# Optimization experiments

Measured on AMD Instinct MI355X. Metric: run time of the kernel, lower is better.

## Reference

```python
import jax, jax.numpy as jnp
import numpy as np

D = 8        # input_path_dim (number of driving channels / base vector fields)
N = 256      # cde_state_dim
H = 512      # vf_hidden_dim
B = 4096     # batch of evaluation points (vmapped calls)
P = D * (D - 1) // 2            # number of depth-2 Lyndon brackets (i<j)
M = D + P                       # total brackets = depth-2 Lyndon basis size
_II, _JJ = np.triu_indices(D, k=1)   # Lyndon words (i,j), i<j


def _mlp_fields(h, W1, b1, W2, b2, W3, b3, Wo, bo):
    # eqx.nn.MLP(in=N, out=D*N, width=H, depth=3, softplus hidden, tanh final)
    x = jax.nn.softplus(W1 @ h + b1)
    x = jax.nn.softplus(W2 @ x + b2)
    x = jax.nn.softplus(W3 @ x + b3)
    return jnp.tanh(Wo @ x + bo).reshape(D, N)   # V_i(h), i=1..D


def setup_inputs() -> dict:
    key = jax.random.key(0)
    ks = jax.random.split(key, 10)

    def lin(kw, kb, out_dim, in_dim):
        lim = 1.0 / np.sqrt(in_dim)
        W = jax.random.uniform(kw, (out_dim, in_dim), minval=-lim, maxval=lim, dtype=jnp.float32)
        b = jax.random.uniform(kb, (out_dim,), minval=-lim, maxval=lim, dtype=jnp.float32)
        return W, b

    W1, b1 = lin(ks[0], ks[1], H, N)
    W2, b2 = lin(ks[2], ks[3], H, H)
    W3, b3 = lin(ks[4], ks[5], H, H)
    Wo, bo = lin(ks[6], ks[7], D * N, H)
    h = jax.random.normal(ks[8], (B, N), dtype=jnp.float32)
    primitive_signature = jax.random.normal(ks[9], (B, M), dtype=jnp.float32) * 0.1
    return {
        "h": h, "primitive_signature": primitive_signature,
        "W1": W1, "b1": b1, "W2": W2, "b2": b2,
        "W3": W3, "b3": b3, "Wo": Wo, "bo": bo,
    }


def reference(h, primitive_signature, W1, b1, W2, b2, W3, b3, Wo, bo):
    def single(hv, sig):
        F = lambda y: _mlp_fields(y, W1, b1, W2, b2, W3, b3, Wo, bo)  # [D, N]
        V = F(hv)                                                      # level-1 brackets V_i(h)
        # J[k, i] = DV_i(h) @ V_k(h); one jvp per base-field direction
        J = jax.vmap(lambda v: jax.jvp(F, (hv,), (v,))[1])(V)          # [D, D, N]
        # Lyndon lift, depth 2: [V_i, V_j](h) = DV_j V_i - DV_i V_j, i<j
        lvl2 = J[_II, _JJ] - J[_JJ, _II]                               # [P, N]
        brackets = jnp.concatenate([V, lvl2], axis=0)                  # [M, N]
        # log-ODE contraction against primitive log-signature coefficients
        return jnp.einsum("mn,m->n", brackets, sig)                    # [N]

    return jax.vmap(single)(h, primitive_signature)                    # [B, N]
```

## Files before the change

### kernel.cpp

```cpp
#include <hip/hip_runtime.h>
#include <hip/hip_bf16.h>
#include <math.h>

#define MM 36

typedef _Float16 f16;
typedef __attribute__((ext_vector_type(8))) _Float16 f16x8;
typedef __attribute__((ext_vector_type(4))) _Float16 f16x4;
typedef __attribute__((ext_vector_type(4))) float f32x4;

enum { EPI_NONE = 0, EPI_SP = 1, EPI_TANH = 2, EPI_GATE = 3 };

__device__ __forceinline__ void gl_lds16(const f16* g, f16* l) {
    __builtin_amdgcn_global_load_lds(
        (const __attribute__((address_space(1))) void*)g,
        (__attribute__((address_space(3))) void*)l, 16, 0, 0);
}

template <int EPI, int BM, int BN, int TPB, int WN>
__global__ __launch_bounds__(TPB, 4) void gemm16(
    const f16* __restrict__ A, int lda, long aZ,
    const f16* __restrict__ W, int ldw, long wZ,
    const float* __restrict__ bias,
    void* __restrict__ C0v, int ldc, long cZ,
    const f16* __restrict__ G,
    int K, int cshift)
{
    constexpr int WM = TPB / 64 / WN;
    constexpr int FM = BM / (WM * 16);
    constexpr int FN = BN / (WN * 16);
    constexpr int LA = BM * 4 / TPB;
    constexpr int LB = BN * 4 / TPB;

    __shared__ __align__(16) f16 smem[2 * (BM + BN) * 32];
    f16* As0 = smem;
    f16* Ws0 = smem + 2 * BM * 32;

    const int t = threadIdx.x;
    const int z = blockIdx.z;
    A += (size_t)z * aZ;
    W += (size_t)z * wZ;

    const int nxy = gridDim.x * gridDim.y;
    const int orig = blockIdx.x + gridDim.x * blockIdx.y;
    const int q = nxy >> 3, r = nxy & 7;
    const int xcd = orig & 7, idx = orig >> 3;
    const int nid = (xcd < r ? xcd * (q + 1) : r * (q + 1) + (xcd - r) * q) + idx;
    const long rowTile = (long)(nid >> cshift) * BM;
    const long colTile = (long)(nid & ((1 << cshift) - 1)) * BN;

    const int wave = t >> 6;
    const int lane = t & 63;
    const int wr = (wave / WN) * (FM * 16);
    const int wc = (wave % WN) * (FN * 16);
    const int lr = lane & 15;
    const int lk = lane >> 4;

    const f16* Ag = A + (rowTile + (t >> 2)) * lda + (t & 3) * 8;
    const f16* Wg = W + (colTile + (t >> 2)) * ldw + (t & 3) * 8;

    f32x4 acc[FM][FN];
    const f32x4 zero = {0.f, 0.f, 0.f, 0.f};
#pragma unroll
    for (int m = 0; m < FM; ++m)
#pragma unroll
        for (int n = 0; n < FN; ++n) acc[m][n] = zero;

    const int nt = K >> 5;

    auto stage = [&](int buf, int k0) {
#pragma unroll
        for (int p = 0; p < LA; ++p)
            gl_lds16(Ag + (long)p * (TPB / 4) * lda + k0, &As0[buf * (BM * 32) + (p * TPB + t) * 8]);
#pragma unroll
        for (int p = 0; p < LB; ++p)
            gl_lds16(Wg + (long)p * (TPB / 4) * ldw + k0, &Ws0[buf * (BN * 32) + (p * TPB + t) * 8]);
    };

    stage(0, 0);

    for (int ti = 0; ti < nt; ++ti) {
        const int buf = ti & 1;
        __syncthreads();
        if (ti + 1 < nt) stage(buf ^ 1, (ti + 1) << 5);
        f16x8 a[FM], b[FN];
#pragma unroll
        for (int m = 0; m < FM; ++m)
            a[m] = *(const f16x8*)&As0[buf * (BM * 32) + (wr + m * 16 + lr) * 32 + lk * 8];
#pragma unroll
        for (int n = 0; n < FN; ++n)
            b[n] = *(const f16x8*)&Ws0[buf * (BN * 32) + (wc + n * 16 + lr) * 32 + lk * 8];
#pragma unroll
        for (int m = 0; m < FM; ++m)
#pragma unroll
            for (int n = 0; n < FN; ++n)
                acc[m][n] = __builtin_amdgcn_mfma_f32_16x16x32_f16(a[m], b[n], acc[m][n], 0, 0, 0);
    }

    const int erow = t >> 4;
    const int ecq  = (t & 15) * 8;

    __syncthreads();
#pragma unroll
    for (int m = 0; m < FM; ++m) {
#pragma unroll
        for (int n = 0; n < FN; ++n) {
            const int lcol = wc + n * 16 + lr;
            const float bb = bias ? bias[colTile + lcol] : 0.f;
#pragma unroll
            for (int j = 0; j < 4; ++j) {
                const int lrow = wr + m * 16 + lk * 4 + j;
                const int lidx = lrow * BN + (lcol ^ (lk * 16));
                const float x = acc[m][n][j] + bb;
                if constexpr (EPI == EPI_SP) {
                    const float e = __expf(-fabsf(x));
                    smem[lidx] = (f16)(fmaxf(x, 0.f) + __logf(1.f + e));
                } else if constexpr (EPI == EPI_TANH) {
                    const float e2 = __expf(2.f * x);
                    smem[lidx] = (f16)(1.f - 2.f * __builtin_amdgcn_rcpf(e2 + 1.f));
                } else if constexpr (EPI == EPI_GATE) {
                    const long row = rowTile + lrow;
                    const float s = (float)G[(row >> 3) * ldc + colTile + lcol];
                    const float g = 1.f - __expf(-s);
                    smem[lidx] = (f16)(x * g);
                } else {
                    smem[lidx] = (f16)x;
                }
            }
        }
    }
    __syncthreads();
    {
        f16* dst = (EPI == EPI_NONE) ? ((f16*)C0v + (size_t)z * cZ) : (f16*)C0v;
#pragma unroll
        for (int p = 0; p < BM / 16; ++p) {
            const int row = p * 16 + erow;
            const f16x8 v = *(const f16x8*)&smem[row * BN + (ecq ^ (((row >> 2) & 3) * 16))];
            *(f16x8*)&dst[(rowTile + row) * ldc + colTile + ecq] = v;
        }
    }
}

__global__ __launch_bounds__(256) void ktilde16(
    const f16* __restrict__ V, const float* __restrict__ sig,
    f16* __restrict__ T, int b0)
{
    const int bl = blockIdx.x * 4 + (threadIdx.x >> 6);
    const int n0 = (threadIdx.x & 63) * 4;
    const f16* vb = V + (size_t)bl * 2048 + n0;
    float v[8][4];
#pragma unroll
    for (int k = 0; k < 8; ++k) {
        const f16x4 x = *(const f16x4*)&vb[k * 256];
#pragma unroll
        for (int j = 0; j < 4; ++j) v[k][j] = (float)x[j];
    }
    const float* sg = sig + (size_t)(b0 + bl) * MM + 8;
    float s2[28];
#pragma unroll
    for (int p = 0; p < 28; ++p) s2[p] = sg[p];

    f16* tb = T + (size_t)bl * 2048 + n0;
#pragma unroll
    for (int i = 0; i < 8; ++i) {
        float a0 = 0.f, a1 = 0.f, a2 = 0.f, a3 = 0.f;
#pragma unroll
        for (int k = 0; k < 8; ++k) {
            if (k == i) continue;
            const int a = (k < i) ? k : i;
            const int b = (k < i) ? i : k;
            const int p = a * (15 - a) / 2 + (b - a - 1);
            const float c = (k < i) ? s2[p] : -s2[p];
            a0 = fmaf(c, v[k][0], a0); a1 = fmaf(c, v[k][1], a1);
            a2 = fmaf(c, v[k][2], a2); a3 = fmaf(c, v[k][3], a3);
        }
        f16x4 o;
        o[0] = (f16)a0; o[1] = (f16)a1; o[2] = (f16)a2; o[3] = (f16)a3;
        *(f16x4*)&tb[i * 256] = o;
    }
}

__global__ __launch_bounds__(256) void finish16(
    const f16* __restrict__ V, const f16* __restrict__ Oi,
    const float* __restrict__ sig, float* __restrict__ out, int b0, int C)
{
    const int bl = blockIdx.x * 4 + (threadIdx.x >> 6);
    const int n0 = (threadIdx.x & 63) * 4;
    const float* sg = sig + (size_t)(b0 + bl) * MM;
    float a0 = 0.f, a1 = 0.f, a2 = 0.f, a3 = 0.f;
#pragma unroll
    for (int i = 0; i < 8; ++i) {
        const f16x4 vv = *(const f16x4*)&V[(size_t)bl * 2048 + i * 256 + n0];
        const f16x4 oo = *(const f16x4*)&Oi[((size_t)i * C + bl) * 256 + n0];
        const float s = sg[i];
        const float v0 = (float)vv[0], v1 = (float)vv[1];
        const float v2 = (float)vv[2], v3 = (float)vv[3];
        a0 = fmaf(s, v0, a0); a0 = fmaf(1.f - v0 * v0, (float)oo[0], a0);
        a1 = fmaf(s, v1, a1); a1 = fmaf(1.f - v1 * v1, (float)oo[1], a1);
        a2 = fmaf(s, v2, a2); a2 = fmaf(1.f - v2 * v2, (float)oo[2], a2);
        a3 = fmaf(s, v3, a3); a3 = fmaf(1.f - v3 * v3, (float)oo[3], a3);
    }
    float4 ov; ov.x = a0; ov.y = a1; ov.z = a2; ov.w = a3;
    *(float4*)&out[(size_t)(b0 + bl) * 256 + n0] = ov;
}

__global__ __launch_bounds__(256) void cvtW(
    const float* __restrict__ W1, const float* __restrict__ W2,
    const float* __restrict__ W3, const float* __restrict__ Wo,
    f16* __restrict__ o1, f16* __restrict__ o2,
    f16* __restrict__ o3, f16* __restrict__ oo)
{
    long i = (long)blockIdx.x * 256 + threadIdx.x;
    const float* src; f16* dst; long base;
    if (i < 32768)       { src = W1; dst = o1; base = 0; }
    else if (i < 98304)  { src = W2; dst = o2; base = 32768; }
    else if (i < 163840) { src = W3; dst = o3; base = 98304; }
    else                 { src = Wo; dst = oo; base = 163840; }
    i -= base;
    const float4 v = ((const float4*)src)[i];
    f16x4 o;
    o[0] = (f16)v.x; o[1] = (f16)v.y; o[2] = (f16)v.z; o[3] = (f16)v.w;
    ((f16x4*)dst)[i] = o;
}

__global__ __launch_bounds__(256) void cvt16(
    const float* __restrict__ x, f16* __restrict__ y, int n)
{
    const int i = (blockIdx.x * 256 + threadIdx.x) * 4;
    if (i < n) {
        const float4 v = *(const float4*)&x[i];
        f16x4 o;
        o[0] = (f16)v.x; o[1] = (f16)v.y; o[2] = (f16)v.z; o[3] = (f16)v.w;
        *(f16x4*)&y[i] = o;
    }
}

extern "C" void kernel_launch(void* const* d_in, const int* in_sizes, int n_in,
                              void* d_out, int out_size, void* d_ws, size_t ws_size,
                              hipStream_t stream) {
    const float* h   = (const float*)d_in[0];
    const float* sig = (const float*)d_in[1];
    const float* W1  = (const float*)d_in[2];
    const float* b1  = (const float*)d_in[3];
    const float* W2  = (const float*)d_in[4];
    const float* b2  = (const float*)d_in[5];
    const float* W3  = (const float*)d_in[6];
    const float* b3  = (const float*)d_in[7];
    const float* Wo  = (const float*)d_in[8];
    const float* bo  = (const float*)d_in[9];
    float* out = (float*)d_out;

    char* p = (char*)d_ws;
    f16* W1h = (f16*)p; p += (size_t)512 * 256 * 2;
    f16* W2h = (f16*)p; p += (size_t)512 * 512 * 2;
    f16* W3h = (f16*)p; p += (size_t)512 * 512 * 2;
    f16* Woh = (f16*)p; p += (size_t)2048 * 512 * 2;
    const size_t fixed = (size_t)(p - (char*)d_ws);

    int C = 4096;
    while (C > 128 && fixed + (size_t)C * 28160 > ws_size) C >>= 1;

    f16* h16 = (f16*)p; p += (size_t)C * 256 * 2;
    f16* s1 = (f16*)p;  p += (size_t)C * 512 * 2;
    f16* s2 = (f16*)p;  p += (size_t)C * 512 * 2;
    f16* s3 = (f16*)p;  p += (size_t)C * 512 * 2;
    f16* V  = (f16*)p;  p += (size_t)C * 2048 * 2;
    f16* T  = (f16*)p;  p += (size_t)C * 2048 * 2;
    f16* Ua = (f16*)p;  p += (size_t)C * 4096 * 2;
    f16* Ub = (f16*)p;
    f16* Oi = Ub;

    const dim3 blk(256);
    cvtW<<<dim3(1664), blk, 0, stream>>>(W1, W2, W3, Wo, W1h, W2h, W3h, Woh);

    for (int b0 = 0; b0 < 4096; b0 += C) {
        cvt16<<<dim3(C * 256 / 1024), blk, 0, stream>>>(h + (size_t)b0 * 256, h16, C * 256);
        gemm16<EPI_SP, 64, 128, 256, 4><<<dim3(4, C / 64), blk, 0, stream>>>(
            h16, 256, 0, W1h, 256, 0, b1, s1, 512, 0, nullptr, 256, 2);
        gemm16<EPI_SP, 64, 128, 256, 4><<<dim3(4, C / 64), blk, 0, stream>>>(
            s1, 512, 0, W2h, 512, 0, b2, s2, 512, 0, nullptr, 512, 2);
        gemm16<EPI_SP, 64, 128, 256, 4><<<dim3(4, C / 64), blk, 0, stream>>>(
            s2, 512, 0, W3h, 512, 0, b3, s3, 512, 0, nullptr, 512, 2);
        gemm16<EPI_TANH, 128, 128, 256, 2><<<dim3(16, C / 128), blk, 0, stream>>>(
            s3, 512, 0, Woh, 512, 0, bo, V, 2048, 0, nullptr, 512, 4);
        ktilde16<<<dim3(C / 4), blk, 0, stream>>>(V, sig, T, b0);
        gemm16<EPI_GATE, 128, 128, 256, 2><<<dim3(4, C / 16), blk, 0, stream>>>(
            T, 256, 0, W1h, 256, 0, nullptr, Ua, 512, 0, s1, 256, 2);
        gemm16<EPI_GATE, 128, 128, 256, 2><<<dim3(4, C / 16), blk, 0, stream>>>(
            Ua, 512, 0, W2h, 512, 0, nullptr, Ub, 512, 0, s2, 512, 2);
        gemm16<EPI_GATE, 128, 128, 256, 2><<<dim3(4, C / 16), blk, 0, stream>>>(
            Ub, 512, 0, W3h, 512, 0, nullptr, Ua, 512, 0, s3, 512, 2);
        gemm16<EPI_NONE, 128, 128, 256, 2><<<dim3(2, C / 128, 8), blk, 0, stream>>>(
            Ua, 4096, 512, Woh, 512, (long)256 * 512, nullptr, Oi, 256, (long)C * 256,
            nullptr, 512, 1);
        finish16<<<dim3(C / 4), blk, 0, stream>>>(V, Oi, sig, out, b0, C);
    }
}
```

Before: 170.9 us.

## Add 256x256-tile triple-buffered 8-wave GEMM for gated tangent layers

Adds a dedicated 512-thread GEMM kernel with 256x256 output tiles, a three-stage LDS ring fed by direct global-to-LDS loads, XCD-aware block remapping, and s_setprio around the MFMA bursts. It is used for the three gated JVP hidden-layer GEMMs, which have 8x the batch rows. The goal is more operand reuse per tile and better overlap of loads with MFMA work. In exchange it uses 96 KB of LDS and many accumulator registers, which lowers occupancy. The epilogue is split into two halves so the C tile can be staged through LDS.

```diff
diff --git a/kernel.cpp b/kernel.cpp
--- a/kernel.cpp
+++ b/kernel.cpp
@@ -15,6 +15,138 @@
     __builtin_amdgcn_global_load_lds(
         (const __attribute__((address_space(1))) void*)g,
         (__attribute__((address_space(3))) void*)l, 16, 0, 0);
+}
+
+__global__ __launch_bounds__(512, 2) void gemm8p(
+    const f16* __restrict__ A, int lda,
+    const f16* __restrict__ W, int ldw,
+    f16* __restrict__ C, int ldc,
+    const f16* __restrict__ G,
+    int K)
+{
+    __shared__ __align__(16) f16 smem[49152];
+    f16* bufA = smem;
+    f16* bufB = smem + 24576;
+
+    const int t = threadIdx.x;
+    const int nxy = gridDim.x * gridDim.y;
+    const int orig = blockIdx.x + gridDim.x * blockIdx.y;
+    const int q = nxy >> 3, r = nxy & 7;
+    const int xcd = orig & 7, idx = orig >> 3;
+    const int nid = (xcd < r ? xcd * (q + 1) : r * (q + 1) + (xcd - r) * q) + idx;
+    const long rowTile = (long)(nid >> 1) * 256;
+    const long colTile = (long)(nid & 1) * 256;
+
+    const int wave = t >> 6;
+    const int lane = t & 63;
+    const int wm = wave >> 2;
+    const int wn = wave & 3;
+    const int lr = lane & 15;
+    const int lk = lane >> 4;
+    const int rq = lk ^ (lr & 3);
+
+    const int srow = t >> 2;
+    const int skq  = t & 3;
+
+    f32x4 acc[8][4];
+    const f32x4 zero = {0.f, 0.f, 0.f, 0.f};
+#pragma unroll
+    for (int m = 0; m < 8; ++m)
+#pragma unroll
+        for (int n = 0; n < 4; ++n) acc[m][n] = zero;
+
+    const int nt = K >> 5;
+
+    auto stageA = [&](int buf, int tk) {
+        const int k0 = tk << 5;
+#pragma unroll
+        for (int p = 0; p < 2; ++p) {
+            const int row = srow + p * 128;
+            gl_lds16(A + (rowTile + row) * (long)lda + k0 + (skq ^ (row & 3)) * 8,
+                     &bufA[buf * 8192 + (p * 512 + t) * 8]);
+        }
+    };
+    auto stageB = [&](int buf, int tk) {
+        const int k0 = tk << 5;
+#pragma unroll
+        for (int p = 0; p < 2; ++p) {
+            const int row = srow + p * 128;
+            gl_lds16(W + (colTile + row) * (long)ldw + k0 + (skq ^ (row & 3)) * 8,
+                     &bufB[buf * 8192 + (p * 512 + t) * 8]);
+        }
+    };
+
+    stageA(0, 0); stageB(0, 0);
+    stageA(1, 1); stageB(1, 1);
+    asm volatile("s_waitcnt vmcnt(4)" ::: "memory");
+    __builtin_amdgcn_s_barrier();
+
+    for (int tk = 0; tk < nt; ++tk) {
+        const int cb = tk % 3;
+        const int sb = (tk + 2) % 3;
+        const f16* At = &bufA[cb * 8192];
+        const f16* Bt = &bufB[cb * 8192];
+        f16x8 a[4], b[4];
+#pragma unroll
+        for (int m = 0; m < 4; ++m)
+            a[m] = *(const f16x8*)&At[(wm * 128 + m * 16 + lr) * 32 + rq * 8];
+#pragma unroll
+        for (int n = 0; n < 4; ++n)
+            b[n] = *(const f16x8*)&Bt[(wn * 64 + n * 16 + lr) * 32 + rq * 8];
+        if (tk + 2 < nt) stageA(sb, tk + 2);
+        __builtin_amdgcn_s_setprio(1);
+#pragma unroll
+        for (int m = 0; m < 4; ++m)
+#pragma unroll
+            for (int n = 0; n < 4; ++n)
+                acc[m][n] = __builtin_amdgcn_mfma_f32_16x16x32_f16(a[m], b[n], acc[m][n], 0, 0, 0);
+        __builtin_amdgcn_s_setprio(0);
+#pragma unroll
+        for (int m = 0; m < 4; ++m)
+            a[m] = *(const f16x8*)&At[(wm * 128 + (m + 4) * 16 + lr) * 32 + rq * 8];
+        if (tk + 2 < nt) stageB(sb, tk + 2);
+        __builtin_amdgcn_s_setprio(1);
+#pragma unroll
+        for (int m = 0; m < 4; ++m)
+#pragma unroll
+            for (int n = 0; n < 4; ++n)
+                acc[m + 4][n] = __builtin_amdgcn_mfma_f32_16x16x32_f16(a[m], b[n], acc[m + 4][n], 0, 0, 0);
+        __builtin_amdgcn_s_setprio(0);
+        if (tk + 1 < nt) {
+            if (tk + 2 < nt) asm volatile("s_waitcnt vmcnt(4)" ::: "memory");
+            else             asm volatile("s_waitcnt vmcnt(0)" ::: "memory");
+            __builtin_amdgcn_s_barrier();
+        }
+    }
+
+#pragma unroll
+    for (int half = 0; half < 2; ++half) {
+        __builtin_amdgcn_s_barrier();
+        if (wm == half) {
+#pragma unroll
+            for (int m = 0; m < 8; ++m)
+#pragma unroll
+                for (int n = 0; n < 4; ++n)
+#pragma unroll
+                    for (int j = 0; j < 4; ++j) {
+                        const int lrow = m * 16 + lk * 4 + j;
+                        const int lcol = wn * 64 + n * 16 + lr;
+                        const long row = rowTile + half * 128 + lrow;
+                        const float s = (float)G[(row >> 3) * ldc + colTile + lcol];
+                        const float g = 1.f - __expf(-s);
+                        smem[lrow * 256 + (lcol ^ (lk * 16))] = (f16)(acc[m][n][j] * g);
+                    }
+        }
+        __builtin_amdgcn_s_barrier();
+#pragma unroll
+        for (int p = 0; p < 8; ++p) {
+            const int c = p * 512 + t;
+            const int rl = c >> 5;
+            const int c16 = (c & 31) * 8;
+            const f16x8 v = *(const f16x8*)&smem[rl * 256 + (c16 ^ (((rl >> 2) & 3) * 16))];
+            *(f16x8*)&C[(rowTile + half * 128 + rl) * ldc + colTile + c16] = v;
+        }
+    }
 }
 
 template <int EPI, int BM, int BN, int TPB, int WN>
@@ -121,8 +253,7 @@
                 } else if constexpr (EPI == EPI_GATE) {
                     const long row = rowTile + lrow;
                     const float s = (float)G[(row >> 3) * ldc + colTile + lcol];
-                    const float g = 1.f - __expf(-s);
-                    smem[lidx] = (f16)(x * g);
+                    smem[lidx] = (f16)(x * (1.f - __expf(-s)));
                 } else {
                     smem[lidx] = (f16)x;
                 }
@@ -271,6 +402,7 @@
     f16* Oi = Ub;
 
     const dim3 blk(256);
+    const dim3 blk8(512);
     cvtW<<<dim3(1664), blk, 0, stream>>>(W1, W2, W3, Wo, W1h, W2h, W3h, Woh);
 
     for (int b0 = 0; b0 < 4096; b0 += C) {
@@ -284,12 +416,12 @@
         gemm16<EPI_TANH, 128, 128, 256, 2><<<dim3(16, C / 128), blk, 0, stream>>>(
             s3, 512, 0, Woh, 512, 0, bo, V, 2048, 0, nullptr, 512, 4);
         ktilde16<<<dim3(C / 4), blk, 0, stream>>>(V, sig, T, b0);
-        gemm16<EPI_GATE, 128, 128, 256, 2><<<dim3(4, C / 16), blk, 0, stream>>>(
-            T, 256, 0, W1h, 256, 0, nullptr, Ua, 512, 0, s1, 256, 2);
-        gemm16<EPI_GATE, 128, 128, 256, 2><<<dim3(4, C / 16), blk, 0, stream>>>(
-            Ua, 512, 0, W2h, 512, 0, nullptr, Ub, 512, 0, s2, 512, 2);
-        gemm16<EPI_GATE, 128, 128, 256, 2><<<dim3(4, C / 16), blk, 0, stream>>>(
-            Ub, 512, 0, W3h, 512, 0, nullptr, Ua, 512, 0, s3, 512, 2);
+        gemm8p<<<dim3(2, C * 8 / 256), blk8, 0, stream>>>(
+            T, 256, W1h, 256, Ua, 512, s1, 256);
+        gemm8p<<<dim3(2, C * 8 / 256), blk8, 0, stream>>>(
+            Ua, 512, W2h, 512, Ub, 512, s2, 512);
+        gemm8p<<<dim3(2, C * 8 / 256), blk8, 0, stream>>>(
+            Ub, 512, W3h, 512, Ua, 512, s3, 512);
         gemm16<EPI_NONE, 128, 128, 256, 2><<<dim3(2, C / 128, 8), blk, 0, stream>>>(
             Ua, 4096, 512, Woh, 512, (long)256 * 512, nullptr, Oi, 256, (long)C * 256,
             nullptr, 512, 1);
```

Result: faster. 163.5 us (-4.3%).

## Triple-buffer GEMM pipeline with LDS swizzle, bigger gate tiles, fuse finish via atomics

Applied to the files above, without the earlier changes.

The GEMM kernel moves from double to triple buffering, waiting with explicit vmcnt counts and a single barrier per k-step. It adds an XOR swizzle on the LDS staging layout and raises MFMA priority with setprio. The gated tangent GEMMs switch to 256x128 tiles with 512 threads. The separate finish kernel is removed: ktilde writes the level-1 term directly, and the last batched GEMM folds the (1-V^2)*O contribution into the output with float atomicAdd across the 8 z-slices. The atomics add contention and make the summation order nondeterministic, in exchange for dropping the Oi round trip and one launch.

```diff
diff --git a/kernel.cpp b/kernel.cpp
--- a/kernel.cpp
+++ b/kernel.cpp
@@ -9,7 +9,7 @@
 typedef __attribute__((ext_vector_type(4))) _Float16 f16x4;
 typedef __attribute__((ext_vector_type(4))) float f32x4;
 
-enum { EPI_NONE = 0, EPI_SP = 1, EPI_TANH = 2, EPI_GATE = 3 };
+enum { EPI_NONE = 0, EPI_SP = 1, EPI_TANH = 2, EPI_GATE = 3, EPI_DIAG = 4 };
 
 __device__ __forceinline__ void gl_lds16(const f16* g, f16* l) {
     __builtin_amdgcn_global_load_lds(
@@ -18,12 +18,15 @@
 }
 
 template <int EPI, int BM, int BN, int TPB, int WN>
-__global__ __launch_bounds__(TPB, 4) void gemm16(
+__global__ __launch_bounds__(TPB, (163840 / (3 * (BM + BN) * 64)) * TPB / 256) void gemmCV(
     const f16* __restrict__ A, int lda, long aZ,
     const f16* __restrict__ W, int ldw, long wZ,
     const float* __restrict__ bias,
-    void* __restrict__ C0v, int ldc, long cZ,
+    f16* __restrict__ C, int ldc, long cZ,
     const f16* __restrict__ G,
+    const f16* __restrict__ Vp,
+    float* __restrict__ outp,
+    int b0,
     int K, int cshift)
 {
     constexpr int WM = TPB / 64 / WN;
@@ -31,15 +34,17 @@
     constexpr int FN = BN / (WN * 16);
     constexpr int LA = BM * 4 / TPB;
     constexpr int LB = BN * 4 / TPB;
-
-    __shared__ __align__(16) f16 smem[2 * (BM + BN) * 32];
-    f16* As0 = smem;
-    f16* Ws0 = smem + 2 * BM * 32;
+    constexpr int L  = LA + LB;
+
+    __shared__ __align__(16) f16 smem[3 * (BM + BN) * 32];
+    f16* bufA = smem;
+    f16* bufB = smem + 3 * BM * 32;
 
     const int t = threadIdx.x;
     const int z = blockIdx.z;
     A += (size_t)z * aZ;
     W += (size_t)z * wZ;
+    C += (size_t)z * cZ;
 
     const int nxy = gridDim.x * gridDim.y;
     const int orig = blockIdx.x + gridDim.x * blockIdx.y;
@@ -55,9 +60,9 @@
     const int wc = (wave % WN) * (FN * 16);
     const int lr = lane & 15;
     const int lk = lane >> 4;
-
-    const f16* Ag = A + (rowTile + (t >> 2)) * lda + (t & 3) * 8;
-    const f16* Wg = W + (colTile + (t >> 2)) * ldw + (t & 3) * 8;
+    const int rq = lk ^ (lr & 3);
+    const int srow = t >> 2;
+    const int skq  = t & 3;
 
     f32x4 acc[FM][FN];
     const f32x4 zero = {0.f, 0.f, 0.f, 0.f};
@@ -68,37 +73,57 @@
 
     const int nt = K >> 5;
 
-    auto stage = [&](int buf, int k0) {
-#pragma unroll
-        for (int p = 0; p < LA; ++p)
-            gl_lds16(Ag + (long)p * (TPB / 4) * lda + k0, &As0[buf * (BM * 32) + (p * TPB + t) * 8]);
-#pragma unroll
-        for (int p = 0; p < LB; ++p)
-            gl_lds16(Wg + (long)p * (TPB / 4) * ldw + k0, &Ws0[buf * (BN * 32) + (p * TPB + t) * 8]);
+    auto stage = [&](int buf, int tk) {
+        const int k0 = tk << 5;
+#pragma unroll
+        for (int p = 0; p < LA; ++p) {
+            const int row = srow + p * (TPB / 4);
+            gl_lds16(A + (rowTile + row) * (long)lda + k0 + (skq ^ (row & 3)) * 8,
+                     &bufA[buf * (BM * 32) + (p * TPB + t) * 8]);
+        }
+#pragma unroll
+        for (int p = 0; p < LB; ++p) {
+            const int row = srow + p * (TPB / 4);
+            gl_lds16(W + (colTile + row) * (long)ldw + k0 + (skq ^ (row & 3)) * 8,
+                     &bufB[buf * (BN * 32) + (p * TPB + t) * 8]);
+        }
     };
+    auto waitL = [&]() {
+        if constexpr (L == 3) asm volatile("s_waitcnt vmcnt(3)" ::: "memory");
+        else if constexpr (L == 4) asm volatile("s_waitcnt vmcnt(4)" ::: "memory");
+        else asm volatile("s_waitcnt vmcnt(0)" ::: "memory");
+    };
 
     stage(0, 0);
-
-    for (int ti = 0; ti < nt; ++ti) {
-        const int buf = ti & 1;
-        __syncthreads();
-        if (ti + 1 < nt) stage(buf ^ 1, (ti + 1) << 5);
+    stage(1, 1);
+    waitL();
+    __builtin_amdgcn_s_barrier();
+
+    for (int tk = 0; tk < nt; ++tk) {
+        const int cb = tk % 3;
+        const f16* At = &bufA[cb * (BM * 32)];
+        const f16* Bt = &bufB[cb * (BN * 32)];
         f16x8 a[FM], b[FN];
 #pragma unroll
         for (int m = 0; m < FM; ++m)
-            a[m] = *(const f16x8*)&As0[buf * (BM * 32) + (wr + m * 16 + lr) * 32 + lk * 8];
+            a[m] = *(const f16x8*)&At[(wr + m * 16 + lr) * 32 + rq * 8];
 #pragma unroll
         for (int n = 0; n < FN; ++n)
-            b[n] = *(const f16x8*)&Ws0[buf * (BN * 32) + (wc + n * 16 + lr) * 32 + lk * 8];
+            b[n] = *(const f16x8*)&Bt[(wc + n * 16 + lr) * 32 + rq * 8];
+        if (tk + 2 < nt) stage((tk + 2) % 3, tk + 2);
+        __builtin_amdgcn_s_setprio(1);
 #pragma unroll
         for (int m = 0; m < FM; ++m)
 #pragma unroll
             for (int n = 0; n < FN; ++n)
                 acc[m][n] = __builtin_amdgcn_mfma_f32_16x16x32_f16(a[m], b[n], acc[m][n], 0, 0, 0);
-    }
-
-    const int erow = t >> 4;
-    const int ecq  = (t & 15) * 8;
+        __builtin_amdgcn_s_setprio(0);
+        if (tk + 1 < nt) {
+            if (tk + 2 < nt) waitL();
+            else asm volatile("s_waitcnt vmcnt(0)" ::: "memory");
+            __builtin_amdgcn_s_barrier();
+        }
+    }
 
     __syncthreads();
 #pragma unroll
@@ -121,8 +146,7 @@
                 } else if constexpr (EPI == EPI_GATE) {
                     const long row = rowTile + lrow;
                     const float s = (float)G[(row >> 3) * ldc + colTile + lcol];
-                    const float g = 1.f - __expf(-s);
-                    smem[lidx] = (f16)(x * g);
+                    smem[lidx] = (f16)(x * (1.f - __expf(-s)));
                 } else {
                     smem[lidx] = (f16)x;
                 }
@@ -130,20 +154,30 @@
         }
     }
     __syncthreads();
-    {
-        f16* dst = (EPI == EPI_NONE) ? ((f16*)C0v + (size_t)z * cZ) : (f16*)C0v;
-#pragma unroll
-        for (int p = 0; p < BM / 16; ++p) {
-            const int row = p * 16 + erow;
-            const f16x8 v = *(const f16x8*)&smem[row * BN + (ecq ^ (((row >> 2) & 3) * 16))];
-            *(f16x8*)&dst[(rowTile + row) * ldc + colTile + ecq] = v;
+#pragma unroll
+    for (int p = 0; p < BM * BN / (8 * TPB); ++p) {
+        const int c = p * TPB + t;
+        const int rl = c / (BN / 8);
+        const int c16 = (c % (BN / 8)) * 8;
+        const f16x8 v = *(const f16x8*)&smem[rl * BN + (c16 ^ (((rl >> 2) & 3) * 16))];
+        if constexpr (EPI == EPI_DIAG) {
+            const long row = rowTile + rl;
+            const f16x8 v8 = *(const f16x8*)&Vp[row * 2048 + z * 256 + colTile + c16];
+            float* op = &outp[(size_t)(b0 + row) * 256 + colTile + c16];
+#pragma unroll
+            for (int e = 0; e < 8; ++e) {
+                const float vv = (float)v8[e];
+                atomicAdd(&op[e], (1.f - vv * vv) * (float)v[e]);
+            }
+        } else {
+            *(f16x8*)&C[(rowTile + rl) * ldc + colTile + c16] = v;
         }
     }
 }
 
 __global__ __launch_bounds__(256) void ktilde16(
     const f16* __restrict__ V, const float* __restrict__ sig,
-    f16* __restrict__ T, int b0)
+    f16* __restrict__ T, float* __restrict__ out, int b0)
 {
     const int bl = blockIdx.x * 4 + (threadIdx.x >> 6);
     const int n0 = (threadIdx.x & 63) * 4;
@@ -155,10 +189,23 @@
 #pragma unroll
         for (int j = 0; j < 4; ++j) v[k][j] = (float)x[j];
     }
-    const float* sg = sig + (size_t)(b0 + bl) * MM + 8;
-    float s2[28];
-#pragma unroll
-    for (int p = 0; p < 28; ++p) s2[p] = sg[p];
+    const float* sg = sig + (size_t)(b0 + bl) * MM;
+    float s1v[8], s2[28];
+#pragma unroll
+    for (int k = 0; k < 8; ++k) s1v[k] = sg[k];
+#pragma unroll
+    for (int p = 0; p < 28; ++p) s2[p] = sg[8 + p];
+
+    {
+        float b0v = 0.f, b1v = 0.f, b2v = 0.f, b3v = 0.f;
+#pragma unroll
+        for (int k = 0; k < 8; ++k) {
+            b0v = fmaf(s1v[k], v[k][0], b0v); b1v = fmaf(s1v[k], v[k][1], b1v);
+            b2v = fmaf(s1v[k], v[k][2], b2v); b3v = fmaf(s1v[k], v[k][3], b3v);
+        }
+        float4 ov; ov.x = b0v; ov.y = b1v; ov.z = b2v; ov.w = b3v;
+        *(float4*)&out[(size_t)(b0 + bl) * 256 + n0] = ov;
+    }
 
     f16* tb = T + (size_t)bl * 2048 + n0;
 #pragma unroll
@@ -178,30 +225,6 @@
         o[0] = (f16)a0; o[1] = (f16)a1; o[2] = (f16)a2; o[3] = (f16)a3;
         *(f16x4*)&tb[i * 256] = o;
     }
-}
-
-__global__ __launch_bounds__(256) void finish16(
-    const f16* __restrict__ V, const f16* __restrict__ Oi,
-    const float* __restrict__ sig, float* __restrict__ out, int b0, int C)
-{
-    const int bl = blockIdx.x * 4 + (threadIdx.x >> 6);
-    const int n0 = (threadIdx.x & 63) * 4;
-    const float* sg = sig + (size_t)(b0 + bl) * MM;
-    float a0 = 0.f, a1 = 0.f, a2 = 0.f, a3 = 0.f;
-#pragma unroll
-    for (int i = 0; i < 8; ++i) {
-        const f16x4 vv = *(const f16x4*)&V[(size_t)bl * 2048 + i * 256 + n0];
-        const f16x4 oo = *(const f16x4*)&Oi[((size_t)i * C + bl) * 256 + n0];
-        const float s = sg[i];
-        const float v0 = (float)vv[0], v1 = (float)vv[1];
-        const float v2 = (float)vv[2], v3 = (float)vv[3];
-        a0 = fmaf(s, v0, a0); a0 = fmaf(1.f - v0 * v0, (float)oo[0], a0);
-        a1 = fmaf(s, v1, a1); a1 = fmaf(1.f - v1 * v1, (float)oo[1], a1);
-        a2 = fmaf(s, v2, a2); a2 = fmaf(1.f - v2 * v2, (float)oo[2], a2);
-        a3 = fmaf(s, v3, a3); a3 = fmaf(1.f - v3 * v3, (float)oo[3], a3);
-    }
-    float4 ov; ov.x = a0; ov.y = a1; ov.z = a2; ov.w = a3;
-    *(float4*)&out[(size_t)(b0 + bl) * 256 + n0] = ov;
 }
 
 __global__ __launch_bounds__(256) void cvtW(
@@ -268,31 +291,30 @@
     f16* T  = (f16*)p;  p += (size_t)C * 2048 * 2;
     f16* Ua = (f16*)p;  p += (size_t)C * 4096 * 2;
     f16* Ub = (f16*)p;
-    f16* Oi = Ub;
 
     const dim3 blk(256);
+    const dim3 blk5(512);
     cvtW<<<dim3(1664), blk, 0, stream>>>(W1, W2, W3, Wo, W1h, W2h, W3h, Woh);
 
     for (int b0 = 0; b0 < 4096; b0 += C) {
         cvt16<<<dim3(C * 256 / 1024), blk, 0, stream>>>(h + (size_t)b0 * 256, h16, C * 256);
-        gemm16<EPI_SP, 64, 128, 256, 4><<<dim3(4, C / 64), blk, 0, stream>>>(
-            h16, 256, 0, W1h, 256, 0, b1, s1, 512, 0, nullptr, 256, 2);
-        gemm16<EPI_SP, 64, 128, 256, 4><<<dim3(4, C / 64), blk, 0, stream>>>(
-            s1, 512, 0, W2h, 512, 0, b2, s2, 512, 0, nullptr, 512, 2);
-        gemm16<EPI_SP, 64, 128, 256, 4><<<dim3(4, C / 64), blk, 0, stream>>>(
-            s2, 512, 0, W3h, 512, 0, b3, s3, 512, 0, nullptr, 512, 2);
-        gemm16<EPI_TANH, 128, 128, 256, 2><<<dim3(16, C / 128), blk, 0, stream>>>(
-            s3, 512, 0, Woh, 512, 0, bo, V, 2048, 0, nullptr, 512, 4);
-        ktilde16<<<dim3(C / 4), blk, 0, stream>>>(V, sig, T, b0);
-        gemm16<EPI_GATE, 128, 128, 256, 2><<<dim3(4, C / 16), blk, 0, stream>>>(
-            T, 256, 0, W1h, 256, 0, nullptr, Ua, 512, 0, s1, 256, 2);
-        gemm16<EPI_GATE, 128, 128, 256, 2><<<dim3(4, C / 16), blk, 0, stream>>>(
-            Ua, 512, 0, W2h, 512, 0, nullptr, Ub, 512, 0, s2, 512, 2);
-        gemm16<EPI_GATE, 128, 128, 256, 2><<<dim3(4, C / 16), blk, 0, stream>>>(
-            Ub, 512, 0, W3h, 512, 0, nullptr, Ua, 512, 0, s3, 512, 2);
-        gemm16<EPI_NONE, 128, 128, 256, 2><<<dim3(2, C / 128, 8), blk, 0, stream>>>(
-            Ua, 4096, 512, Woh, 512, (long)256 * 512, nullptr, Oi, 256, (long)C * 256,
-            nullptr, 512, 1);
-        finish16<<<dim3(C / 4), blk, 0, stream>>>(V, Oi, sig, out, b0, C);
-    }
-}
+        gemmCV<EPI_SP, 64, 128, 256, 4><<<dim3(4, C / 64), blk, 0, stream>>>(
+            h16, 256, 0, W1h, 256, 0, b1, s1, 512, 0, nullptr, nullptr, nullptr, 0, 256, 2);
+        gemmCV<EPI_SP, 64, 128, 256, 4><<<dim3(4, C / 64), blk, 0, stream>>>(
+            s1, 512, 0, W2h, 512, 0, b2, s2, 512, 0, nullptr, nullptr, nullptr, 0, 512, 2);
+        gemmCV<EPI_SP, 64, 128, 256, 4><<<dim3(4, C / 64), blk, 0, stream>>>(
+            s2, 512, 0, W3h, 512, 0, b3, s3, 512, 0, nullptr, nullptr, nullptr, 0, 512, 2);
+        gemmCV<EPI_TANH, 128, 128, 256, 2><<<dim3(16, C / 128), blk, 0, stream>>>(
+            s3, 512, 0, Woh, 512, 0, bo, V, 2048, 0, nullptr, nullptr, nullptr, 0, 512, 4);
+        ktilde16<<<dim3(C / 4), blk, 0, stream>>>(V, sig, T, out, b0);
+        gemmCV<EPI_GATE, 256, 128, 512, 2><<<dim3(4, C * 8 / 256), blk5, 0, stream>>>(
+            T, 256, 0, W1h, 256, 0, nullptr, Ua, 512, 0, s1, nullptr, nullptr, 0, 256, 2);
+        gemmCV<EPI_GATE, 256, 128, 512, 2><<<dim3(4, C * 8 / 256), blk5, 0, stream>>>(
+            Ua, 512, 0, W2h, 512, 0, nullptr, Ub, 512, 0, s2, nullptr, nullptr, 0, 512, 2);
+        gemmCV<EPI_GATE, 256, 128, 512, 2><<<dim3(4, C * 8 / 256), blk5, 0, stream>>>(
+            Ub, 512, 0, W3h, 512, 0, nullptr, Ua, 512, 0, s3, nullptr, nullptr, 0, 512, 2);
+        gemmCV<EPI_DIAG, 128, 128, 256, 2><<<dim3(2, C / 128, 8), blk, 0, stream>>>(
+            Ua, 4096, 512, Woh, 512, (long)256 * 512, nullptr, nullptr, 256, 0,
+            nullptr, V, out, b0, 512, 1);
+    }
+}
```

Result: slower. 385.9 us (+125.9%).
